# Optimization experiments

Hardware: AMD Instinct MI355X
Metric: run time of the kernel (lower is better)

## Reference

```python
import jax, jax.numpy as jnp
import numpy as np

EPS = 0.97  # ContrastLoss eps
T = 0.07    # temperature

def _embed(x, W, b):
    # Linear + L2 normalize (Normalize(power=2))
    h = x @ W.T + b                     # [B, feat_dim]
    norm = jnp.sqrt(jnp.sum(h * h, axis=1, keepdims=True))
    return h / norm

def setup_inputs() -> dict:
    key = jax.random.key(0)
    ks = jax.random.split(key, 7)
    B, S, Td, F = 8192, 2048, 2048, 128
    return {
        "f_s": jax.random.normal(ks[0], (B, S), jnp.float32),
        "f_t": jax.random.normal(ks[1], (B, Td), jnp.float32),
        "y": jax.random.randint(ks[2], (B,), 0, 100, jnp.int64),
        "W_s": jax.random.normal(ks[3], (F, S), jnp.float32) * 0.02,
        "b_s": jax.random.normal(ks[4], (F,), jnp.float32) * 0.02,
        "W_t": jax.random.normal(ks[5], (F, Td), jnp.float32) * 0.02,
        "b_t": jax.random.normal(ks[6], (F,), jnp.float32) * 0.02,
    }

def reference(f_s, f_t, y, W_s, b_s, W_t, b_t):
    fs = _embed(f_s, W_s, b_s)
    ft = _embed(f_t, W_t, b_t)
    # CRDLoss re-normalizes (idempotent, kept for fidelity)
    fs = fs / jnp.linalg.norm(fs, axis=1, keepdims=True)
    ft = ft / jnp.linalg.norm(ft, axis=1, keepdims=True)
    bsz = fs.shape[0]
    x = jnp.exp((fs @ ft.T) / T)  # [B, B] exponentiated similarities
    same = y[None, :] == y[:, None]        # y_expand == y_expand.T
    diag = jnp.eye(bsz, dtype=bool)
    pos_mask = same & ~diag
    neg_mask = ~same & ~diag
    # masked log-ratio sums instead of dynamic-shape gathers
    log_D1 = jnp.log(x / (x + EPS))
    log_D0 = jnp.log(EPS / (x + EPS))
    loss = -(jnp.sum(jnp.where(pos_mask, log_D1, 0.0))
             + jnp.sum(jnp.where(neg_mask, log_D0, 0.0))) / bsz
    return loss
```

## Files before the change

kernel.cpp:

```cpp
#include <hip/hip_runtime.h>
#include <math.h>


typedef _Float16 half_t;
typedef half_t halfx4 __attribute__((ext_vector_type(4)));
typedef half_t halfx8 __attribute__((ext_vector_type(8)));
typedef float f32x4 __attribute__((ext_vector_type(4)));

#define B_TOT   8192
#define K_EMB   2048
#define F_DIM   128
#define INV_T   14.285714285714286f
#define EPS_C   0.97f
#define LOG_EPS (-0.030459207485f)

__global__ __launch_bounds__(256) void embed_kernel(
    const float* __restrict__ Xs, const float* __restrict__ Xt,
    const float* __restrict__ Ws, const float* __restrict__ Wt,
    const float* __restrict__ bs, const float* __restrict__ bt,
    half_t* __restrict__ outs, half_t* __restrict__ outt)
{
    const float* X; const float* W; const float* bias; half_t* out;
    if (blockIdx.y == 0) { X = Xs; W = Ws; bias = bs; out = outs; }
    else                 { X = Xt; W = Wt; bias = bt; out = outt; }

    __shared__ half_t As[2][64][72];
    __shared__ half_t Bs[2][128][72];
    __shared__ float  biasS[128];
    __shared__ float  redS[64][2];
    __shared__ float  invS[64];

    const int tid = threadIdx.x;
    const int r0  = blockIdx.x * 64;
    if (tid < 128) biasS[tid] = bias[tid];

    const int lane = tid & 63;
    const int w    = tid >> 6;
    const int wm   = w >> 1, wn = w & 1;
    const int l16  = lane & 15, lhi = lane >> 4;

    f32x4 acc[2][4];
    for (int im = 0; im < 2; ++im)
        for (int in = 0; in < 4; ++in)
            acc[im][in] = f32x4{0.f, 0.f, 0.f, 0.f};

    const int ar[4] = { (tid) >> 4, (tid + 256) >> 4, (tid + 512) >> 4, (tid + 768) >> 4 };
    const int ak = (tid & 15) * 4;

    float4 na[4], nb[8];

#pragma unroll
    for (int i = 0; i < 4; ++i)
        na[i] = *(const float4*)(X + (size_t)(r0 + ar[i]) * K_EMB + ak);
#pragma unroll
    for (int i = 0; i < 8; ++i)
        nb[i] = *(const float4*)(W + (size_t)((tid + i * 256) >> 4) * K_EMB + ak);
#pragma unroll
    for (int i = 0; i < 4; ++i) {
        halfx4 h4 = {(half_t)na[i].x, (half_t)na[i].y, (half_t)na[i].z, (half_t)na[i].w};
        *(halfx4*)&As[0][ar[i]][ak] = h4;
    }
#pragma unroll
    for (int i = 0; i < 8; ++i) {
        halfx4 h4 = {(half_t)nb[i].x, (half_t)nb[i].y, (half_t)nb[i].z, (half_t)nb[i].w};
        *(halfx4*)&Bs[0][(tid + i * 256) >> 4][ak] = h4;
    }
    __syncthreads();

    for (int it = 0; it < 32; ++it) {
        const int cur = it & 1;
        if (it < 31) {
            const int kb = (it + 1) * 64;
#pragma unroll
            for (int i = 0; i < 4; ++i)
                na[i] = *(const float4*)(X + (size_t)(r0 + ar[i]) * K_EMB + kb + ak);
#pragma unroll
            for (int i = 0; i < 8; ++i)
                nb[i] = *(const float4*)(W + (size_t)((tid + i * 256) >> 4) * K_EMB + kb + ak);
        }
#pragma unroll
        for (int kk = 0; kk < 2; ++kk) {
            halfx8 a[2], b[4];
#pragma unroll
            for (int im = 0; im < 2; ++im)
                a[im] = *(const halfx8*)&As[cur][wm * 32 + im * 16 + l16][kk * 32 + lhi * 8];
#pragma unroll
            for (int in = 0; in < 4; ++in)
                b[in] = *(const halfx8*)&Bs[cur][wn * 64 + in * 16 + l16][kk * 32 + lhi * 8];
#pragma unroll
            for (int im = 0; im < 2; ++im)
#pragma unroll
                for (int in = 0; in < 4; ++in)
                    acc[im][in] = __builtin_amdgcn_mfma_f32_16x16x32_f16(
                        a[im], b[in], acc[im][in], 0, 0, 0);
        }
        if (it < 31) {
            const int nxt = cur ^ 1;
#pragma unroll
            for (int i = 0; i < 4; ++i) {
                halfx4 h4 = {(half_t)na[i].x, (half_t)na[i].y, (half_t)na[i].z, (half_t)na[i].w};
                *(halfx4*)&As[nxt][ar[i]][ak] = h4;
            }
#pragma unroll
            for (int i = 0; i < 8; ++i) {
                halfx4 h4 = {(half_t)nb[i].x, (half_t)nb[i].y, (half_t)nb[i].z, (half_t)nb[i].w};
                *(halfx4*)&Bs[nxt][(tid + i * 256) >> 4][ak] = h4;
            }
        }
        __syncthreads();
    }

    float h[2][4][4];
    float psum[2][4];
    for (int im = 0; im < 2; ++im)
        for (int reg = 0; reg < 4; ++reg) {
            float p = 0.f;
            for (int in = 0; in < 4; ++in) {
                int col = wn * 64 + in * 16 + l16;
                float v = acc[im][in][reg] + biasS[col];
                h[im][in][reg] = v;
                p += v * v;
            }
            p += __shfl_xor(p, 1);
            p += __shfl_xor(p, 2);
            p += __shfl_xor(p, 4);
            p += __shfl_xor(p, 8);
            psum[im][reg] = p;
        }
    if (l16 == 0)
        for (int im = 0; im < 2; ++im)
            for (int reg = 0; reg < 4; ++reg)
                redS[wm * 32 + im * 16 + lhi * 4 + reg][wn] = psum[im][reg];
    __syncthreads();
    if (tid < 64) invS[tid] = rsqrtf(redS[tid][0] + redS[tid][1]);
    __syncthreads();

    for (int im = 0; im < 2; ++im)
        for (int in = 0; in < 4; ++in)
            for (int reg = 0; reg < 4; ++reg) {
                int row = wm * 32 + im * 16 + lhi * 4 + reg;
                int col = wn * 64 + in * 16 + l16;
                out[(size_t)(r0 + row) * F_DIM + col] =
                    (half_t)(h[im][in][reg] * invS[row]);
            }
}

__global__ __launch_bounds__(256) void loss_kernel(
    const half_t* __restrict__ FS, const half_t* __restrict__ FT,
    const int* __restrict__ y, double* __restrict__ partials)
{
    __shared__ uint4 As4[128 * 8];
    __shared__ uint4 Bs4[128 * 8];
    __shared__ int   yrl[128], ycl[128];
    __shared__ float wsum[4];

    const int tid = threadIdx.x;
    const int i0  = blockIdx.x * 128;
    const int j0  = blockIdx.y * 128;

    if (tid < 128) yrl[tid] = y[i0 + tid];
    else           ycl[tid - 128] = y[j0 + tid - 128];

    const int lane = tid & 63;
    const int w    = tid >> 6;
    const int wm   = w >> 1, wn = w & 1;
    const int l16  = lane & 15, lhi = lane >> 4;

#pragma unroll
    for (int i = 0; i < 4; ++i) {
        int f = tid + i * 256;
        int row = f >> 3, c = f & 7;
        As4[row * 8 + (c ^ (row & 7))] = *(const uint4*)(FS + (size_t)(i0 + row) * F_DIM + c * 8);
    }
#pragma unroll
    for (int i = 0; i < 4; ++i) {
        int f = tid + i * 256;
        int row = f >> 3, c = f & 7;
        Bs4[row * 8 + (c ^ (row & 7))] = *(const uint4*)(FT + (size_t)(j0 + row) * F_DIM + c * 8);
    }
    __syncthreads();

    f32x4 acc[4][4];
    for (int im = 0; im < 4; ++im)
        for (int in = 0; in < 4; ++in)
            acc[im][in] = f32x4{0.f, 0.f, 0.f, 0.f};

    for (int kc = 0; kc < 2; ++kc) {
#pragma unroll
        for (int kk = 0; kk < 2; ++kk) {
            halfx8 a[4], b[4];
#pragma unroll
            for (int im = 0; im < 4; ++im) {
                int r = wm * 64 + im * 16 + l16;
                a[im] = *(const halfx8*)&As4[r * 8 + ((kk * 4 + lhi) ^ (r & 7))];
            }
#pragma unroll
            for (int in = 0; in < 4; ++in) {
                int r = wn * 64 + in * 16 + l16;
                b[in] = *(const halfx8*)&Bs4[r * 8 + ((kk * 4 + lhi) ^ (r & 7))];
            }
#pragma unroll
            for (int im = 0; im < 4; ++im)
#pragma unroll
                for (int in = 0; in < 4; ++in)
                    acc[im][in] = __builtin_amdgcn_mfma_f32_16x16x32_f16(
                        a[im], b[in], acc[im][in], 0, 0, 0);
        }
        if (kc == 0) {
            __syncthreads();
#pragma unroll
            for (int i = 0; i < 4; ++i) {
                int f = tid + i * 256;
                int row = f >> 3, c = f & 7;
                As4[row * 8 + (c ^ (row & 7))] =
                    *(const uint4*)(FS + (size_t)(i0 + row) * F_DIM + 64 + c * 8);
            }
#pragma unroll
            for (int i = 0; i < 4; ++i) {
                int f = tid + i * 256;
                int row = f >> 3, c = f & 7;
                Bs4[row * 8 + (c ^ (row & 7))] =
                    *(const uint4*)(FT + (size_t)(j0 + row) * F_DIM + 64 + c * 8);
            }
            __syncthreads();
        }
    }

    float local = 0.f;
    for (int im = 0; im < 4; ++im) {
        for (int reg = 0; reg < 4; ++reg) {
            int il = wm * 64 + im * 16 + lhi * 4 + reg;
            int yi = yrl[il];
            int gi = i0 + il;
            for (int in = 0; in < 4; ++in) {
                int jl = wn * 64 + in * 16 + l16;
                float s  = acc[im][in][reg];
                float sT = s * INV_T;
                float e  = __expf(sT);
                float l  = __logf(e + EPS_C);
                float term = (yi == ycl[jl]) ? (sT - l) : (LOG_EPS - l);
                if (gi != (j0 + jl)) local += term;
            }
        }
    }
    for (int m = 1; m < 64; m <<= 1) local += __shfl_xor(local, m);
    if (lane == 0) wsum[w] = local;
    __syncthreads();
    if (tid == 0)
        partials[blockIdx.y * gridDim.x + blockIdx.x] =
            ((double)wsum[0] + (double)wsum[1]) + ((double)wsum[2] + (double)wsum[3]);
}

__global__ __launch_bounds__(256) void finalize_kernel(
    const double* __restrict__ partials, float* __restrict__ out)
{
    __shared__ double sh[4];
    double loc = 0.0;
    for (int i = threadIdx.x; i < 4096; i += 256) loc += partials[i];
    for (int m = 1; m < 64; m <<= 1) loc += __shfl_xor(loc, m);
    int lane = threadIdx.x & 63, w = threadIdx.x >> 6;
    if (lane == 0) sh[w] = loc;
    __syncthreads();
    if (threadIdx.x == 0)
        out[0] = (float)(-(sh[0] + sh[1] + sh[2] + sh[3]) / (double)B_TOT);
}

extern "C" void kernel_launch(void* const* d_in, const int* in_sizes, int n_in,
                              void* d_out, int out_size, void* d_ws, size_t ws_size,
                              hipStream_t stream)
{
    const size_t WS_NEEDED = (64 << 10) + (4 << 20);
    if (ws_size < WS_NEEDED) return;

    const float* f_s = (const float*)d_in[0];
    const float* f_t = (const float*)d_in[1];
    const int*   y   = (const int*)d_in[2];
    const float* W_s = (const float*)d_in[3];
    const float* b_s = (const float*)d_in[4];
    const float* W_t = (const float*)d_in[5];
    const float* b_t = (const float*)d_in[6];
    float* out = (float*)d_out;

    char* ws = (char*)d_ws;
    double* partials = (double*)ws;
    half_t* fs = (half_t*)(ws + (64 << 10));
    half_t* ft = (half_t*)(ws + (64 << 10) + (2 << 20));

    embed_kernel<<<dim3(128, 2), 256, 0, stream>>>(f_s, f_t, W_s, W_t, b_s, b_t, fs, ft);
    loss_kernel<<<dim3(64, 64), 256, 0, stream>>>(fs, ft, y, partials);
    finalize_kernel<<<1, 256, 0, stream>>>(partials, out);
    (void)in_sizes; (void)n_in; (void)out_size;
}
```

Before: 215.9 us.

## Pre-convert weights to fp16 and halve embed row tile to double grid

Adds a small kernel that converts both weight matrices to fp16 once per call, so the embed kernel loads half-precision W tiles straight into shared memory with no per-block conversion. The embed tile shrinks from 64 to 32 rows, which doubles the grid from 256 to 512 blocks for better CU occupancy on a machine with many CUs. The cost is one extra launch plus a write and reread of the fp16 weights, and each block now reuses its W tile across fewer rows, so total W traffic goes up.

```diff
diff --git a/kernel.cpp b/kernel.cpp
--- a/kernel.cpp
+++ b/kernel.cpp
@@ -14,56 +14,65 @@
 #define EPS_C   0.97f
 #define LOG_EPS (-0.030459207485f)
 
+__global__ __launch_bounds__(256) void cvt_w_kernel(
+    const float* __restrict__ Ws, const float* __restrict__ Wt,
+    half_t* __restrict__ Ws16, half_t* __restrict__ Wt16)
+{
+    const float* src = blockIdx.y ? Wt : Ws;
+    half_t* dst = blockIdx.y ? Wt16 : Ws16;
+    int pos4 = blockIdx.x * 256 + threadIdx.x;
+    float4 v = *(const float4*)(src + (size_t)pos4 * 4);
+    halfx4 h4 = {(half_t)v.x, (half_t)v.y, (half_t)v.z, (half_t)v.w};
+    *(halfx4*)(dst + (size_t)pos4 * 4) = h4;
+}
+
 __global__ __launch_bounds__(256) void embed_kernel(
     const float* __restrict__ Xs, const float* __restrict__ Xt,
-    const float* __restrict__ Ws, const float* __restrict__ Wt,
+    const half_t* __restrict__ Ws16, const half_t* __restrict__ Wt16,
     const float* __restrict__ bs, const float* __restrict__ bt,
     half_t* __restrict__ outs, half_t* __restrict__ outt)
 {
-    const float* X; const float* W; const float* bias; half_t* out;
-    if (blockIdx.y == 0) { X = Xs; W = Ws; bias = bs; out = outs; }
-    else                 { X = Xt; W = Wt; bias = bt; out = outt; }
-
-    __shared__ half_t As[2][64][72];
+    const float* X; const half_t* W16; const float* bias; half_t* out;
+    if (blockIdx.y == 0) { X = Xs; W16 = Ws16; bias = bs; out = outs; }
+    else                 { X = Xt; W16 = Wt16; bias = bt; out = outt; }
+
+    __shared__ half_t As[2][32][72];
     __shared__ half_t Bs[2][128][72];
     __shared__ float  biasS[128];
-    __shared__ float  redS[64][2];
-    __shared__ float  invS[64];
+    __shared__ float  redS[32][2];
+    __shared__ float  invS[32];
 
     const int tid = threadIdx.x;
-    const int r0  = blockIdx.x * 64;
+    const int r0  = blockIdx.x * 32;
     if (tid < 128) biasS[tid] = bias[tid];
 
     const int lane = tid & 63;
     const int w    = tid >> 6;
-    const int wm   = w >> 1, wn = w & 1;
+    const int wm   = w & 1, wn = w >> 1;
     const int l16  = lane & 15, lhi = lane >> 4;
 
-    f32x4 acc[2][4];
-    for (int im = 0; im < 2; ++im)
-        for (int in = 0; in < 4; ++in)
-            acc[im][in] = f32x4{0.f, 0.f, 0.f, 0.f};
-
-    const int ar[4] = { (tid) >> 4, (tid + 256) >> 4, (tid + 512) >> 4, (tid + 768) >> 4 };
-    const int ak = (tid & 15) * 4;
-
-    float4 na[4], nb[8];
-
+    f32x4 acc[4];
+    for (int in = 0; in < 4; ++in) acc[in] = f32x4{0.f, 0.f, 0.f, 0.f};
+
+    const int ar0 = tid >> 4, ar1 = (tid + 256) >> 4;
+    const int akq = (tid & 15) * 4;
+    const int bc  = (tid & 7) * 8;
+
+    float4 na[2]; uint4 nb[4];
+
+    na[0] = *(const float4*)(X + (size_t)(r0 + ar0) * K_EMB + akq);
+    na[1] = *(const float4*)(X + (size_t)(r0 + ar1) * K_EMB + akq);
 #pragma unroll
     for (int i = 0; i < 4; ++i)
-        na[i] = *(const float4*)(X + (size_t)(r0 + ar[i]) * K_EMB + ak);
-#pragma unroll
-    for (int i = 0; i < 8; ++i)
-        nb[i] = *(const float4*)(W + (size_t)((tid + i * 256) >> 4) * K_EMB + ak);
-#pragma unroll
-    for (int i = 0; i < 4; ++i) {
-        halfx4 h4 = {(half_t)na[i].x, (half_t)na[i].y, (half_t)na[i].z, (half_t)na[i].w};
-        *(halfx4*)&As[0][ar[i]][ak] = h4;
-    }
-#pragma unroll
-    for (int i = 0; i < 8; ++i) {
-        halfx4 h4 = {(half_t)nb[i].x, (half_t)nb[i].y, (half_t)nb[i].z, (half_t)nb[i].w};
-        *(halfx4*)&Bs[0][(tid + i * 256) >> 4][ak] = h4;
+        nb[i] = *(const uint4*)(W16 + (size_t)((tid + i * 256) >> 3) * K_EMB + bc);
+    {
+        halfx4 h0 = {(half_t)na[0].x, (half_t)na[0].y, (half_t)na[0].z, (half_t)na[0].w};
+        halfx4 h1 = {(half_t)na[1].x, (half_t)na[1].y, (half_t)na[1].z, (half_t)na[1].w};
+        *(halfx4*)&As[0][ar0][akq] = h0;
+        *(halfx4*)&As[0][ar1][akq] = h1;
+#pragma unroll
+        for (int i = 0; i < 4; ++i)
+            *(uint4*)&Bs[0][(tid + i * 256) >> 3][bc] = nb[i];
     }
     __syncthreads();
 
@@ -71,78 +80,70 @@
         const int cur = it & 1;
         if (it < 31) {
             const int kb = (it + 1) * 64;
+            na[0] = *(const float4*)(X + (size_t)(r0 + ar0) * K_EMB + kb + akq);
+            na[1] = *(const float4*)(X + (size_t)(r0 + ar1) * K_EMB + kb + akq);
 #pragma unroll
             for (int i = 0; i < 4; ++i)
-                na[i] = *(const float4*)(X + (size_t)(r0 + ar[i]) * K_EMB + kb + ak);
-#pragma unroll
-            for (int i = 0; i < 8; ++i)
-                nb[i] = *(const float4*)(W + (size_t)((tid + i * 256) >> 4) * K_EMB + kb + ak);
+                nb[i] = *(const uint4*)(W16 + (size_t)((tid + i * 256) >> 3) * K_EMB + kb + bc);
         }
 #pragma unroll
         for (int kk = 0; kk < 2; ++kk) {
-            halfx8 a[2], b[4];
-#pragma unroll
-            for (int im = 0; im < 2; ++im)
-                a[im] = *(const halfx8*)&As[cur][wm * 32 + im * 16 + l16][kk * 32 + lhi * 8];
+            halfx8 a, b[4];
+            a = *(const halfx8*)&As[cur][wm * 16 + l16][kk * 32 + lhi * 8];
 #pragma unroll
             for (int in = 0; in < 4; ++in)
                 b[in] = *(const halfx8*)&Bs[cur][wn * 64 + in * 16 + l16][kk * 32 + lhi * 8];
 #pragma unroll
-            for (int im = 0; im < 2; ++im)
-#pragma unroll
-                for (int in = 0; in < 4; ++in)
-                    acc[im][in] = __builtin_amdgcn_mfma_f32_16x16x32_f16(
-                        a[im], b[in], acc[im][in], 0, 0, 0);
+            for (int in = 0; in < 4; ++in)
+                acc[in] = __builtin_amdgcn_mfma_f32_16x16x32_f16(a, b[in], acc[in], 0, 0, 0);
         }
         if (it < 31) {
             const int nxt = cur ^ 1;
-#pragma unroll
-            for (int i = 0; i < 4; ++i) {
-                halfx4 h4 = {(half_t)na[i].x, (half_t)na[i].y, (half_t)na[i].z, (half_t)na[i].w};
-                *(halfx4*)&As[nxt][ar[i]][ak] = h4;
-            }
-#pragma unroll
-            for (int i = 0; i < 8; ++i) {
-                halfx4 h4 = {(half_t)nb[i].x, (half_t)nb[i].y, (half_t)nb[i].z, (half_t)nb[i].w};
-                *(halfx4*)&Bs[nxt][(tid + i * 256) >> 4][ak] = h4;
-            }
+            halfx4 h0 = {(half_t)na[0].x, (half_t)na[0].y, (half_t)na[0].z, (half_t)na[0].w};
+            halfx4 h1 = {(half_t)na[1].x, (half_t)na[1].y, (half_t)na[1].z, (half_t)na[1].w};
+            *(halfx4*)&As[nxt][ar0][akq] = h0;
+            *(halfx4*)&As[nxt][ar1][akq] = h1;
+#pragma unroll
+            for (int i = 0; i < 4; ++i)
+                *(uint4*)&Bs[nxt][(tid + i * 256) >> 3][bc] = nb[i];
         }
         __syncthreads();
     }
 
-    float h[2][4][4];
-    float psum[2][4];
-    for (int im = 0; im < 2; ++im)
+    float h[4][4];
+    float psum[4];
+#pragma unroll
+    for (int reg = 0; reg < 4; ++reg) {
+        float p = 0.f;
+#pragma unroll
+        for (int in = 0; in < 4; ++in) {
+            int col = wn * 64 + in * 16 + l16;
+            float v = acc[in][reg] + biasS[col];
+            h[in][reg] = v;
+            p += v * v;
+        }
+        p += __shfl_xor(p, 1);
+        p += __shfl_xor(p, 2);
+        p += __shfl_xor(p, 4);
+        p += __shfl_xor(p, 8);
+        psum[reg] = p;
+    }
+    if (l16 == 0)
+#pragma unroll
+        for (int reg = 0; reg < 4; ++reg)
+            redS[wm * 16 + lhi * 4 + reg][wn] = psum[reg];
+    __syncthreads();
+    if (tid < 32) invS[tid] = rsqrtf(redS[tid][0] + redS[tid][1]);
+    __syncthreads();
+
+#pragma unroll
+    for (int in = 0; in < 4; ++in)
+#pragma unroll
         for (int reg = 0; reg < 4; ++reg) {
-            float p = 0.f;
-            for (int in = 0; in < 4; ++in) {
-                int col = wn * 64 + in * 16 + l16;
-                float v = acc[im][in][reg] + biasS[col];
-                h[im][in][reg] = v;
-                p += v * v;
-            }
-            p += __shfl_xor(p, 1);
-            p += __shfl_xor(p, 2);
-            p += __shfl_xor(p, 4);
-            p += __shfl_xor(p, 8);
-            psum[im][reg] = p;
-        }
-    if (l16 == 0)
-        for (int im = 0; im < 2; ++im)
-            for (int reg = 0; reg < 4; ++reg)
-                redS[wm * 32 + im * 16 + lhi * 4 + reg][wn] = psum[im][reg];
-    __syncthreads();
-    if (tid < 64) invS[tid] = rsqrtf(redS[tid][0] + redS[tid][1]);
-    __syncthreads();
-
-    for (int im = 0; im < 2; ++im)
-        for (int in = 0; in < 4; ++in)
-            for (int reg = 0; reg < 4; ++reg) {
-                int row = wm * 32 + im * 16 + lhi * 4 + reg;
-                int col = wn * 64 + in * 16 + l16;
-                out[(size_t)(r0 + row) * F_DIM + col] =
-                    (half_t)(h[im][in][reg] * invS[row]);
-            }
+            int row = wm * 16 + lhi * 4 + reg;
+            int col = wn * 64 + in * 16 + l16;
+            out[(size_t)(r0 + row) * F_DIM + col] = (half_t)(h[in][reg] * invS[row]);
+        }
 }
 
 __global__ __launch_bounds__(256) void loss_kernel(
@@ -269,7 +270,7 @@
                               void* d_out, int out_size, void* d_ws, size_t ws_size,
                               hipStream_t stream)
 {
-    const size_t WS_NEEDED = (64 << 10) + (4 << 20);
+    const size_t WS_NEEDED = (64 << 10) + (4 << 20) + (1 << 20);
     if (ws_size < WS_NEEDED) return;
 
     const float* f_s = (const float*)d_in[0];
@@ -283,10 +284,13 @@
 
     char* ws = (char*)d_ws;
     double* partials = (double*)ws;
-    half_t* fs = (half_t*)(ws + (64 << 10));
-    half_t* ft = (half_t*)(ws + (64 << 10) + (2 << 20));
-
-    embed_kernel<<<dim3(128, 2), 256, 0, stream>>>(f_s, f_t, W_s, W_t, b_s, b_t, fs, ft);
+    half_t* fs   = (half_t*)(ws + (64 << 10));
+    half_t* ft   = (half_t*)(ws + (64 << 10) + (2 << 20));
+    half_t* Ws16 = (half_t*)(ws + (64 << 10) + (4 << 20));
+    half_t* Wt16 = (half_t*)(ws + (64 << 10) + (4 << 20) + (512 << 10));
+
+    cvt_w_kernel<<<dim3(256, 2), 256, 0, stream>>>(W_s, W_t, Ws16, Wt16);
+    embed_kernel<<<dim3(256, 2), 256, 0, stream>>>(f_s, f_t, Ws16, Wt16, b_s, b_t, fs, ft);
     loss_kernel<<<dim3(64, 64), 256, 0, stream>>>(fs, ft, y, partials);
     finalize_kernel<<<1, 256, 0, stream>>>(partials, out);
     (void)in_sizes; (void)n_in; (void)out_size;
```

Result: no change. 215.2 us (-0.3%).
